# Kernel optimization log

Measured on AMD Instinct MI355X. Metric: run time of the kernel, lower is better.

## Reference

```python
import jax, jax.numpy as jnp
import numpy as np

N, E, C, NTT, NMOL = 200000, 1600000, 128, 20000, 2000
EPS = 1e-5


def setup_inputs() -> dict:
    key = jax.random.key(0)
    ks = jax.random.split(key, 32)
    s = 0.05
    d = {}
    d["node_attr"] = jax.random.normal(ks[0], (N, C), jnp.float32)
    d["adj_index"] = jax.random.randint(ks[1], (2, E), 0, N)
    d["adj_value"] = jax.random.uniform(ks[2], (E,), jnp.float32)
    d["tt_node_batch"] = jnp.sort(jax.random.randint(ks[3], (N,), 0, NTT))
    d["tt_graph_batch"] = jnp.sort(jax.random.randint(ks[4], (NTT,), 0, NMOL))
    # GCN layers (2): linear weight/bias
    d["W_gcn"] = jax.random.normal(ks[5], (2, C, C)) * s
    d["b_gcn"] = jnp.zeros((2, C))
    # 8 BatchNorm1d(C): [gcn0, gcn1, tt0, tt1, tt2, mol0, mol1, mol2] (eval mode)
    d["bn_gamma"] = jnp.ones((8, C))
    d["bn_beta"] = jnp.zeros((8, C))
    d["bn_mean"] = jnp.zeros((8, C))
    d["bn_var"] = jnp.ones((8, C))
    # 2 GATConv (tt, mol): bipartite lin_src/lin_dst, att_src/att_dst, bias (heads=1)
    d["gat_Wsrc"] = jax.random.normal(ks[6], (2, C, C)) * s
    d["gat_Wdst"] = jax.random.normal(ks[7], (2, C, C)) * s
    d["gat_asrc"] = jax.random.normal(ks[8], (2, C)) * s
    d["gat_adst"] = jax.random.normal(ks[9], (2, C)) * s
    d["gat_bias"] = jnp.zeros((2, C))
    # 2 GRUCell(C, C)
    d["gru_Wih"] = jax.random.normal(ks[10], (2, 3 * C, C)) * s
    d["gru_Whh"] = jax.random.normal(ks[11], (2, 3 * C, C)) * s
    d["gru_bih"] = jnp.zeros((2, 3 * C))
    d["gru_bhh"] = jnp.zeros((2, 3 * C))
    # predictor: 128 -> 64 (relu) -> 1
    d["pW1"] = jax.random.normal(ks[12], (64, C)) * s
    d["pb1"] = jnp.full((64,), 0.01)
    d["pW2"] = jax.random.normal(ks[13], (1, 64)) * s
    d["pb2"] = jnp.full((1,), 0.01)
    return d


def _bn(x, i, g, b, m, v):
    return (x - m[i]) * (g[i] / jnp.sqrt(v[i] + EPS)) + b[i]


def _spmm(idx, val, x, n):  # out[i] = sum_j A[i,j] x[j]
    return jax.ops.segment_sum(val[:, None] * x[idx[1]], idx[0], num_segments=n)


def _gat(x_src, x_dst, src, dst, nseg, Ws, Wd, a_s, a_d, bias):
    hs = x_src @ Ws.T
    hd = x_dst @ Wd.T
    alpha = jax.nn.leaky_relu(hs @ a_s, 0.01 * 0 + 0.01) if False else None
    a = (hs @ a_s)[src] + (hd @ a_d)[dst]
    a = jnp.where(a > 0, a, 0.01 * a)  # leaky_relu, negative_slope=0.01
    mx = jax.ops.segment_max(a, dst, num_segments=nseg)
    e = jnp.exp(a - mx[dst])
    den = jax.ops.segment_sum(e, dst, num_segments=nseg)
    w = e / den[dst]
    return jax.ops.segment_sum(w[:, None] * hs[src], dst, num_segments=nseg) + bias


def _gru(x, h, Wih, Whh, bih, bhh):
    gi = x @ Wih.T + bih
    gh = h @ Whh.T + bhh
    ir, iz, inn = jnp.split(gi, 3, axis=-1)
    hr, hz, hn = jnp.split(gh, 3, axis=-1)
    r = jax.nn.sigmoid(ir + hr)
    z = jax.nn.sigmoid(iz + hz)
    n = jnp.tanh(inn + r * hn)
    return (1.0 - z) * n + z * h


def _pool_stage(x, seg, nseg, bn_base, gi, bn_gamma, bn_beta, bn_mean, bn_var,
                gat_Wsrc, gat_Wdst, gat_asrc, gat_adst, gat_bias,
                gru_Wih, gru_Whh, gru_bih, gru_bhh):
    x = _bn(x, bn_base, bn_gamma, bn_beta, bn_mean, bn_var)
    mean = jax.ops.segment_sum(x, seg, num_segments=nseg)  # global_add_pool
    mean = _bn(jax.nn.relu(mean), bn_base + 1, bn_gamma, bn_beta, bn_mean, bn_var)
    src = jnp.arange(x.shape[0])
    g = _gat(x, mean, src, seg, nseg, gat_Wsrc[gi], gat_Wdst[gi], gat_asrc[gi], gat_adst[gi], gat_bias[gi])
    g = jax.nn.elu(g)  # dropout p=0.001 is identity in eval
    g = _gru(g, mean, gru_Wih[gi], gru_Whh[gi], gru_bih[gi], gru_bhh[gi])
    return _bn(jax.nn.relu(g), bn_base + 2, bn_gamma, bn_beta, bn_mean, bn_var)


def reference(node_attr, adj_value, W_gcn, b_gcn, bn_gamma, bn_beta, bn_mean, bn_var,
              gat_Wsrc, gat_Wdst, gat_asrc, gat_adst, gat_bias,
              gru_Wih, gru_Whh, gru_bih, gru_bhh, pW1, pb1, pW2, pb2,
              adj_index, tt_node_batch, tt_graph_batch):
    # graph embedder: two GCN layers  x <- relu(BN(A @ (x W^T) + b))
    x = node_attr
    for i in range(2):
        x = _spmm(adj_index, adj_value, x @ W_gcn[i].T, N) + b_gcn[i]
        x = jax.nn.relu(_bn(x, i, bn_gamma, bn_beta, bn_mean, bn_var))
    # tt pooling: nodes -> tt subgraphs
    tt = _pool_stage(x, tt_node_batch, NTT, 2, 0, bn_gamma, bn_beta, bn_mean, bn_var,
                     gat_Wsrc, gat_Wdst, gat_asrc, gat_adst, gat_bias,
                     gru_Wih, gru_Whh, gru_bih, gru_bhh)
    # mol pooling: tt subgraphs -> molecules
    mol = _pool_stage(tt, tt_graph_batch, NMOL, 5, 1, bn_gamma, bn_beta, bn_mean, bn_var,
                      gat_Wsrc, gat_Wdst, gat_asrc, gat_adst, gat_bias,
                      gru_Wih, gru_Whh, gru_bih, gru_bhh)
    # predictor
    h = jax.nn.relu(mol @ pW1.T + pb1)
    return h @ pW2.T + pb2  # [NMOL, 1]
```

## Files before the change

kernel.cpp:

```cpp
#include <hip/hip_runtime.h>
#include <math.h>

#define CCH 128
#define G3  384
#define BN_EPS 1e-5f
#define BSH 9
#define BROWS 512
#define COLBITS 19

typedef __bf16 bf16;
typedef __bf16 bf16x2 __attribute__((ext_vector_type(2)));
typedef __bf16 bf16x4 __attribute__((ext_vector_type(4)));
typedef __bf16 bf16x8 __attribute__((ext_vector_type(8)));
typedef float f32x4 __attribute__((ext_vector_type(4)));

__global__ __launch_bounds__(256) void prep_kernel(
    const float* __restrict__ g, const float* __restrict__ b,
    const float* __restrict__ m, const float* __restrict__ v,
    float* __restrict__ bnsc, float* __restrict__ bnsh,
    const float* __restrict__ Wsrc, const float* __restrict__ Wdst,
    const float* __restrict__ asrc, const float* __restrict__ adst,
    float* __restrict__ vsp, float* __restrict__ vd, float* __restrict__ c0,
    const int* __restrict__ tt_node_batch, int N, int NTT, int* __restrict__ starts_tt,
    const int* __restrict__ tt_graph_batch, int NMOL, int* __restrict__ starts_mol,
    int* __restrict__ bhist,
    const float* __restrict__ Wgcn, bf16* __restrict__ Wgcnb,
    bf16* __restrict__ Wsrcb,
    const float* __restrict__ Wih, bf16* __restrict__ Wihb,
    const float* __restrict__ Whh, bf16* __restrict__ Whhb,
    int B1, int B2, int B3, int B4, int B5, int B6, int B7, int B8)
{
    __shared__ float red[2];
    const int bid = blockIdx.x;
    const int tid = threadIdx.x;
    if (bid < B1) {
        int idx = bid * 256 + tid;
        if (idx < 8 * CCH) {
            float s = g[idx] / sqrtf(v[idx] + BN_EPS);
            bnsc[idx] = s;
            bnsh[idx] = b[idx] - m[idx] * s;
        }
    } else if (bid < B2) {
        int s = bid - B1;
        int which = tid >> 7, k = tid & 127;
        const float* W = (which ? Wdst : Wsrc) + s * CCH * CCH;
        const float* a = (which ? adst : asrc) + s * CCH;
        float acc = 0.f;
        for (int j = 0; j < CCH; ++j) acc += W[j * CCH + k] * a[j];
        if (which) {
            vd[s * CCH + k] = acc;
        } else {
            int l = 2 + 3 * s;
            float scl = g[l * CCH + k] / sqrtf(v[l * CCH + k] + BN_EPS);
            float shf = b[l * CCH + k] - m[l * CCH + k] * scl;
            vsp[s * CCH + k] = acc * scl;
            float p = shf * acc;
            for (int o = 32; o; o >>= 1) p += __shfl_down(p, o);
            if ((k & 63) == 0) red[k >> 6] = p;
        }
        __syncthreads();
        if (tid == 0) c0[s] = red[0] + red[1];
    } else if (bid < B3) {
        int s = (bid - B2) * 256 + tid;
        if (s <= NTT) {
            int lo = 0, hi = N;
            while (lo < hi) { int mid = (lo + hi) >> 1; if (tt_node_batch[mid] < s) lo = mid + 1; else hi = mid; }
            starts_tt[s] = lo;
        }
    } else if (bid < B4) {
        int s = (bid - B3) * 256 + tid;
        if (s <= NMOL) {
            int lo = 0, hi = NTT;
            while (lo < hi) { int mid = (lo + hi) >> 1; if (tt_graph_batch[mid] < s) lo = mid + 1; else hi = mid; }
            starts_mol[s] = lo;
        }
    } else if (bid < B5) {
        bhist[tid] = 0; bhist[tid + 256] = 0;
    } else {
        const float* src; bf16* dst; int u0;
        if (bid < B6)      { src = Wgcn; dst = Wgcnb; u0 = (bid - B5) * 256; }
        else if (bid < B7) { src = Wsrc; dst = Wsrcb; u0 = (bid - B6) * 256; }
        else if (bid < B8) { src = Wih;  dst = Wihb;  u0 = (bid - B7) * 256; }
        else               { src = Whh;  dst = Whhb;  u0 = (bid - B8) * 256; }
        int u = u0 + tid;
        int row = u >> 4, kc = u & 15;
        int bi = row >> 7, nrow = row & 127;
        const float* s = src + (size_t)row * CCH + kc * 8;
        float4 a = *(const float4*)s;
        float4 b4 = *(const float4*)(s + 4);
        bf16x8 o = { (bf16)a.x, (bf16)a.y, (bf16)a.z, (bf16)a.w,
                     (bf16)b4.x, (bf16)b4.y, (bf16)b4.z, (bf16)b4.w };
        *(bf16x8*)&dst[(size_t)bi * 16384 + ((kc * 128 + nrow) << 3)] = o;
    }
}


__global__ __launch_bounds__(256) void bucket_hist_kernel(const int* __restrict__ rows,
                                                          int* __restrict__ bhist, int E)
{
    __shared__ int h[512];
    int t = threadIdx.x;
    h[t] = 0; h[t + 256] = 0;
    __syncthreads();
    int base = blockIdx.x * 4096;
#pragma unroll
    for (int i = 0; i < 16; ++i) {
        int e = base + i * 256 + t;
        if (e < E) atomicAdd(&h[rows[e] >> BSH], 1);
    }
    __syncthreads();
    if (h[t]) atomicAdd(&bhist[t], h[t]);
    if (h[t + 256]) atomicAdd(&bhist[t + 256], h[t + 256]);
}

__global__ __launch_bounds__(256) void bucket_scan_kernel(const int* __restrict__ bhist,
                                                          int* __restrict__ boff, int* __restrict__ bcur,
                                                          int* __restrict__ row_ptr, int NB, int N, int E)
{
    __shared__ int h[512], sx[512], wt[4];
    int t = threadIdx.x;
    h[t] = bhist[t]; h[t + 256] = bhist[t + 256];
    __syncthreads();
    int v0 = h[2 * t], v1 = h[2 * t + 1];
    int s = v0 + v1, incl = s;
    for (int o = 1; o < 64; o <<= 1) { int u = __shfl_up(incl, o); if ((t & 63) >= o) incl += u; }
    if ((t & 63) == 63) wt[t >> 6] = incl;
    __syncthreads();
    int woff = 0, w = t >> 6;
    for (int i = 0; i < w; ++i) woff += wt[i];
    int excl = woff + incl - s;
    sx[2 * t] = excl; sx[2 * t + 1] = excl + v0;
    __syncthreads();
    if (t < NB)       { boff[t] = sx[t];       bcur[t] = sx[t]; }
    if (t + 256 < NB) { boff[t + 256] = sx[t + 256]; bcur[t + 256] = sx[t + 256]; }
    if (t == 0) { boff[NB] = E; row_ptr[N] = E; }
}

__global__ __launch_bounds__(256) void bucket_bin_kernel(
    const int* __restrict__ rows, const int* __restrict__ cols, const float* __restrict__ val,
    int* __restrict__ bcur, int2* __restrict__ bcv, int E)
{
    __shared__ int hist[512], sx[512], cnt[512], gbase[512], wt[4];
    __shared__ int mb[4096];
    __shared__ int2 mcv[4096];
    int t = threadIdx.x;
    hist[t] = 0; hist[t + 256] = 0; cnt[t] = 0; cnt[t + 256] = 0;
    __syncthreads();
    int base = blockIdx.x * 4096;
    int r[16];
#pragma unroll
    for (int i = 0; i < 16; ++i) {
        int e = base + i * 256 + t;
        r[i] = (e < E) ? rows[e] : -1;
        if (r[i] >= 0) atomicAdd(&hist[r[i] >> BSH], 1);
    }
    __syncthreads();
    int v0 = hist[2 * t], v1 = hist[2 * t + 1];
    int s = v0 + v1, incl = s;
    for (int o = 1; o < 64; o <<= 1) { int u = __shfl_up(incl, o); if ((t & 63) >= o) incl += u; }
    if ((t & 63) == 63) wt[t >> 6] = incl;
    __syncthreads();
    int woff = 0, w = t >> 6;
    for (int i = 0; i < w; ++i) woff += wt[i];
    int excl = woff + incl - s;
    sx[2 * t] = excl; sx[2 * t + 1] = excl + v0;
    __syncthreads();
    for (int bb = t; bb < 512; bb += 256)
        if (hist[bb]) gbase[bb] = atomicAdd(&bcur[bb], hist[bb]);
    __syncthreads();
#pragma unroll
    for (int i = 0; i < 16; ++i) {
        if (r[i] < 0) continue;
        int e = base + i * 256 + t;
        int bb = r[i] >> BSH;
        int p = atomicAdd(&cnt[bb], 1);
        int loc = sx[bb] + p;
        mb[loc] = bb;
        int2 cv;
        cv.x = cols[e] | ((r[i] & (BROWS - 1)) << COLBITS);
        cv.y = __float_as_int(val[e]);
        mcv[loc] = cv;
    }
    __syncthreads();
    int Mv = sx[511] + hist[511];
    for (int loc = t; loc < Mv; loc += 256) {
        int bb = mb[loc];
        int gidx = gbase[bb] + (loc - sx[bb]);
        bcv[gidx] = mcv[loc];
    }
}

__global__ __launch_bounds__(256) void bucket_place_kernel(
    const int2* __restrict__ bcv, const int* __restrict__ boff, int* __restrict__ row_ptr,
    int2* __restrict__ cpack, int N)
{
    __shared__ int rcnt[512], sx[512], wt[4];
    int b = blockIdx.x;
    int t = threadIdx.x;
    rcnt[t] = 0; rcnt[t + 256] = 0;
    __syncthreads();
    int rbase = b << BSH;
    int rn = min(BROWS, N - rbase);
    int lo = boff[b], hi = boff[b + 1];
    for (int p = lo + t; p < hi; p += 256)
        atomicAdd(&rcnt[((unsigned)bcv[p].x) >> COLBITS], 1);
    __syncthreads();
    int v0 = rcnt[2 * t], v1 = rcnt[2 * t + 1];
    int s = v0 + v1, incl = s;
    for (int o = 1; o < 64; o <<= 1) { int u = __shfl_up(incl, o); if ((t & 63) >= o) incl += u; }
    if ((t & 63) == 63) wt[t >> 6] = incl;
    __syncthreads();
    int woff = 0, w = t >> 6;
    for (int i = 0; i < w; ++i) woff += wt[i];
    int excl = woff + incl - s;
    sx[2 * t] = excl; sx[2 * t + 1] = excl + v0;
    __syncthreads();
    if (t < rn)       row_ptr[rbase + t] = lo + sx[t];
    if (t + 256 < rn) row_ptr[rbase + t + 256] = lo + sx[t + 256];
    __syncthreads();
    sx[t] += lo; sx[t + 256] += lo;
    __syncthreads();
    for (int p = lo + t; p < hi; p += 256) {
        int2 cv = bcv[p];
        int rin = ((unsigned)cv.x) >> COLBITS;
        int slot = atomicAdd(&sx[rin], 1);
        cv.x &= (1 << COLBITS) - 1;
        cpack[slot] = cv;
    }
}


template<int IN_BF16, int OUT_BF16, int ACT>
__global__ __launch_bounds__(256, 4) void gemm_mfma(
    const void* __restrict__ Xv, const bf16* __restrict__ Wf,
    const float* __restrict__ bias, void* __restrict__ Yv, int M, int Nout)
{
    __shared__ bf16 Xs[128 * 128];
    const int tid = threadIdx.x;
    const int rb = blockIdx.x * 128;
    const int cb = blockIdx.y * 128;
    const bf16* Wfb = Wf + (size_t)cb * CCH;

    if (IN_BF16) {
#pragma unroll
        for (int i = 0; i < 8; ++i) {
            int c = tid + i * 256;
            int r = c >> 4, kc = c & 15;
            int grow = rb + r;
            bf16x8 o = {};
            if (grow < M) o = *(const bf16x8*)&((const bf16*)Xv)[(size_t)grow * CCH + kc * 8];
            *(bf16x8*)&Xs[(r * 16 + (kc ^ (r & 15))) << 3] = o;
        }
    } else {
#pragma unroll
        for (int i = 0; i < 16; ++i) {
            int c = tid + i * 256;
            int r = c >> 5, sub = c & 31;
            int kc = sub >> 1, half = sub & 1;
            int grow = rb + r;
            bf16x4 o = {};
            if (grow < M) {
                float4 xv = *(const float4*)&((const float*)Xv)[(size_t)grow * CCH + kc * 8 + half * 4];
                o[0] = (bf16)xv.x; o[1] = (bf16)xv.y; o[2] = (bf16)xv.z; o[3] = (bf16)xv.w;
            }
            *(bf16x4*)&Xs[((r * 16 + (kc ^ (r & 15))) << 3) + half * 4] = o;
        }
    }
    __syncthreads();

    const int w = tid >> 6, lane = tid & 63;
    const int col16 = lane & 15, quad = lane >> 4;
    const int wm = (w & 1) * 64, wn = (w >> 1) * 64;

    f32x4 acc[4][4] = {};
#pragma unroll
    for (int kk = 0; kk < 4; ++kk) {
        const int kc = kk * 4 + quad;
        bf16x8 bfr[4], af[4];
#pragma unroll
        for (int ni = 0; ni < 4; ++ni)
            bfr[ni] = *(const bf16x8*)&Wfb[(size_t)((kc * 128 + wn + ni * 16 + col16) << 3)];
#pragma unroll
        for (int mi = 0; mi < 4; ++mi) {
            int r = wm + mi * 16 + col16;
            af[mi] = *(const bf16x8*)&Xs[(r * 16 + (kc ^ col16)) << 3];
        }
#pragma unroll
        for (int mi = 0; mi < 4; ++mi)
#pragma unroll
            for (int ni = 0; ni < 4; ++ni)
                acc[mi][ni] = __builtin_amdgcn_mfma_f32_16x16x32_bf16(af[mi], bfr[ni], acc[mi][ni], 0, 0, 0);
    }

#pragma unroll
    for (int mi = 0; mi < 4; ++mi) {
#pragma unroll
        for (int r = 0; r < 4; ++r) {
            int row = rb + wm + mi * 16 + quad * 4 + r;
            if (row >= M) continue;
#pragma unroll
            for (int ni = 0; ni < 4; ++ni) {
                int col = cb + wn + ni * 16 + col16;
                float vv = acc[mi][ni][r];
                if (bias) vv += bias[col];
                if (ACT == 1) vv = vv > 0.f ? vv : expm1f(vv);
                if (OUT_BF16) ((bf16*)Yv)[(size_t)row * Nout + col] = (bf16)vv;
                else          ((float*)Yv)[(size_t)row * Nout + col] = vv;
            }
        }
    }
}

__global__ __launch_bounds__(256, 4) void gemm_dual(
    const float* __restrict__ X0, const bf16* __restrict__ W0,
    const float* __restrict__ b0, float* __restrict__ Y0,
    const float* __restrict__ X1, const bf16* __restrict__ W1,
    const float* __restrict__ b1, float* __restrict__ Y1, int M)
{
    __shared__ bf16 Xs[128 * 128];
    const int tid = threadIdx.x;
    const int rb = blockIdx.x * 128;
    const int yy = blockIdx.y;
    const float* X; const bf16* W; const float* bias; float* Y; int cb;
    if (yy < 3) { X = X0; W = W0; bias = b0; Y = Y0; cb = yy * 128; }
    else        { X = X1; W = W1; bias = b1; Y = Y1; cb = (yy - 3) * 128; }
    const bf16* Wfb = W + (size_t)cb * CCH;

#pragma unroll
    for (int i = 0; i < 16; ++i) {
        int c = tid + i * 256;
        int r = c >> 5, sub = c & 31;
        int kc = sub >> 1, half = sub & 1;
        int grow = rb + r;
        bf16x4 o = {};
        if (grow < M) {
            float4 xv = *(const float4*)&X[(size_t)grow * CCH + kc * 8 + half * 4];
            o[0] = (bf16)xv.x; o[1] = (bf16)xv.y; o[2] = (bf16)xv.z; o[3] = (bf16)xv.w;
        }
        *(bf16x4*)&Xs[((r * 16 + (kc ^ (r & 15))) << 3) + half * 4] = o;
    }
    __syncthreads();

    const int w = tid >> 6, lane = tid & 63;
    const int col16 = lane & 15, quad = lane >> 4;
    const int wm = (w & 1) * 64, wn = (w >> 1) * 64;

    f32x4 acc[4][4] = {};
#pragma unroll
    for (int kk = 0; kk < 4; ++kk) {
        const int kc = kk * 4 + quad;
        bf16x8 bfr[4], af[4];
#pragma unroll
        for (int ni = 0; ni < 4; ++ni)
            bfr[ni] = *(const bf16x8*)&Wfb[(size_t)((kc * 128 + wn + ni * 16 + col16) << 3)];
#pragma unroll
        for (int mi = 0; mi < 4; ++mi) {
            int r = wm + mi * 16 + col16;
            af[mi] = *(const bf16x8*)&Xs[(r * 16 + (kc ^ col16)) << 3];
        }
#pragma unroll
        for (int mi = 0; mi < 4; ++mi)
#pragma unroll
            for (int ni = 0; ni < 4; ++ni)
                acc[mi][ni] = __builtin_amdgcn_mfma_f32_16x16x32_bf16(af[mi], bfr[ni], acc[mi][ni], 0, 0, 0);
    }

#pragma unroll
    for (int mi = 0; mi < 4; ++mi) {
#pragma unroll
        for (int r = 0; r < 4; ++r) {
            int row = rb + wm + mi * 16 + quad * 4 + r;
            if (row >= M) continue;
#pragma unroll
            for (int ni = 0; ni < 4; ++ni) {
                int col = cb + wn + ni * 16 + col16;
                Y[(size_t)row * G3 + col] = acc[mi][ni][r] + bias[col];
            }
        }
    }
}

template<int SCORES>
__global__ __launch_bounds__(256) void spmm_csr_kernel(
    const int* __restrict__ row_ptr, const int2* __restrict__ cpack,
    const bf16* __restrict__ Xin, bf16* __restrict__ Y,
    const float* __restrict__ bvec, const float* __restrict__ sc, const float* __restrict__ sh,
    const float* __restrict__ vsp, const float* __restrict__ c0p, float* __restrict__ scores,
    int Nrow)
{
    int gid = blockIdx.x * 256 + threadIdx.x;
    int row = gid >> 4;
    if (row >= Nrow) return;
    int l8 = (gid & 15) << 3;
    int st = row_ptr[row], en = row_ptr[row + 1];
    float acc[8] = {};
    int j = st;
    for (; j + 4 <= en; j += 4) {
        int2 p0 = cpack[j], p1 = cpack[j + 1], p2 = cpack[j + 2], p3 = cpack[j + 3];
        bf16x8 x0 = *(const bf16x8*)&Xin[(size_t)p0.x * CCH + l8];
        bf16x8 x1 = *(const bf16x8*)&Xin[(size_t)p1.x * CCH + l8];
        bf16x8 x2 = *(const bf16x8*)&Xin[(size_t)p2.x * CCH + l8];
        bf16x8 x3 = *(const bf16x8*)&Xin[(size_t)p3.x * CCH + l8];
        float v0 = __int_as_float(p0.y), v1 = __int_as_float(p1.y);
        float v2 = __int_as_float(p2.y), v3 = __int_as_float(p3.y);
#pragma unroll
        for (int q = 0; q < 8; ++q)
            acc[q] += v0 * (float)x0[q] + v1 * (float)x1[q] + v2 * (float)x2[q] + v3 * (float)x3[q];
    }
    if (j + 2 <= en) {
        int2 p0 = cpack[j], p1 = cpack[j + 1];
        bf16x8 x0 = *(const bf16x8*)&Xin[(size_t)p0.x * CCH + l8];
        bf16x8 x1 = *(const bf16x8*)&Xin[(size_t)p1.x * CCH + l8];
        float v0 = __int_as_float(p0.y), v1 = __int_as_float(p1.y);
#pragma unroll
        for (int q = 0; q < 8; ++q) acc[q] += v0 * (float)x0[q] + v1 * (float)x1[q];
        j += 2;
    }
    if (j < en) {
        int2 p0 = cpack[j];
        bf16x8 x0 = *(const bf16x8*)&Xin[(size_t)p0.x * CCH + l8];
        float v0 = __int_as_float(p0.y);
#pragma unroll
        for (int q = 0; q < 8; ++q) acc[q] += v0 * (float)x0[q];
    }
    float o[8];
    bf16x8 ov;
#pragma unroll
    for (int q = 0; q < 8; ++q) {
        o[q] = fmaxf((acc[q] + bvec[l8 + q]) * sc[l8 + q] + sh[l8 + q], 0.f);
        ov[q] = (bf16)o[q];
    }
    *(bf16x8*)&Y[(size_t)row * CCH + l8] = ov;
    if (SCORES) {
        float p = 0.f;
#pragma unroll
        for (int q = 0; q < 8; ++q) p += o[q] * vsp[l8 + q];
        for (int d = 8; d; d >>= 1) p += __shfl_down(p, d, 16);
        if ((gid & 15) == 0) scores[row] = p + c0p[0];
    }
}

__global__ __launch_bounds__(128) void segstage_kernel(
    const bf16* __restrict__ X, const float* __restrict__ sarr, const int* __restrict__ starts,
    const float* __restrict__ sc2, const float* __restrict__ sh2,
    const float* __restrict__ sc3, const float* __restrict__ sh3,
    const float* __restrict__ vd, float* __restrict__ mean, float* __restrict__ upool)
{
    __shared__ float red[2];
    __shared__ float adsh;
    int t = blockIdx.x;
    int c = threadIdx.x;
    int st = starts[t], en = starts[t + 1];
    float sum = 0.f;
    for (int i = st; i < en; ++i) sum += (float)X[(size_t)i * CCH + c];
    float cnt = (float)(en - st);
    float poolb = fmaxf(sum * sc2[c] + cnt * sh2[c], 0.f);
    float mv = poolb * sc3[c] + sh3[c];
    mean[(size_t)t * CCH + c] = mv;
    float p = mv * vd[c];
    for (int o = 32; o; o >>= 1) p += __shfl_down(p, o);
    if ((c & 63) == 0) red[c >> 6] = p;
    __syncthreads();
    if (c == 0) adsh = red[0] + red[1];
    __syncthreads();
    if (en == st) { upool[(size_t)t * CCH + c] = 0.f; return; }
    float adt = adsh;
    float lm = -3.0e38f;
    for (int i = st + c; i < en; i += 128) {
        float a = sarr[i] + adt;
        a = a > 0.f ? a : 0.01f * a;
        lm = fmaxf(lm, a);
    }
    for (int o = 32; o; o >>= 1) lm = fmaxf(lm, __shfl_down(lm, o));
    if ((c & 63) == 0) red[c >> 6] = lm;
    __syncthreads();
    float m = fmaxf(red[0], red[1]);
    float u = 0.f, den = 0.f;
    for (int i = st; i < en; ++i) {
        float a = sarr[i] + adt;
        a = a > 0.f ? a : 0.01f * a;
        float e = __expf(a - m);
        den += e;
        u += e * (float)X[(size_t)i * CCH + c];
    }
    upool[(size_t)t * CCH + c] = (u / den) * sc2[c] + sh2[c];
}

__global__ __launch_bounds__(256) void gru_kernel(
    const float* __restrict__ giM, const float* __restrict__ ghM, const float* __restrict__ mean,
    const float* __restrict__ sc4, const float* __restrict__ sh4,
    bf16* __restrict__ out,
    const float* __restrict__ vsp2, const float* __restrict__ c02, float* __restrict__ scores,
    int total)
{
    __shared__ float sred[4];
    int idx = blockIdx.x * 256 + threadIdx.x;
    bool ok = idx < total;
    int t = idx >> 7, c = idx & 127;
    float o = 0.f;
    if (ok) {
        size_t b = (size_t)t * G3;
        float ir = giM[b + c],  iz = giM[b + 128 + c], inn = giM[b + 256 + c];
        float hr = ghM[b + c],  hz = ghM[b + 128 + c], hn  = ghM[b + 256 + c];
        float r = 1.f / (1.f + __expf(-(ir + hr)));
        float z = 1.f / (1.f + __expf(-(iz + hz)));
        float nn = tanhf(inn + r * hn);
        float h = (1.f - z) * nn + z * mean[idx];
        h = fmaxf(h, 0.f);
        o = h * sc4[c] + sh4[c];
        out[idx] = (bf16)o;
    }
    float p = ok ? o * vsp2[c] : 0.f;
    for (int d = 32; d; d >>= 1) p += __shfl_down(p, d);
    int w = threadIdx.x >> 6;
    if ((threadIdx.x & 63) == 0) sred[w] = p;
    __syncthreads();
    if (threadIdx.x == 0 && ok)   scores[t] = sred[0] + sred[1] + c02[0];
    if (threadIdx.x == 128 && ok) scores[t] = sred[2] + sred[3] + c02[0];
}

__global__ __launch_bounds__(256) void gru_pred_kernel(
    const float* __restrict__ giM, const float* __restrict__ ghM, const float* __restrict__ mean,
    const float* __restrict__ sc4, const float* __restrict__ sh4,
    const float* __restrict__ pW1, const float* __restrict__ pb1,
    const float* __restrict__ pW2, const float* __restrict__ pb2,
    float* __restrict__ out, int nseg)
{
    __shared__ float row[2][CCH];
    int half = threadIdx.x >> 7;
    int c = threadIdx.x & 127;
    int t = blockIdx.x * 2 + half;
    bool ok = t < nseg;
    float o = 0.f;
    if (ok) {
        size_t b = (size_t)t * G3;
        float ir = giM[b + c],  iz = giM[b + 128 + c], inn = giM[b + 256 + c];
        float hr = ghM[b + c],  hz = ghM[b + 128 + c], hn  = ghM[b + 256 + c];
        float r = 1.f / (1.f + __expf(-(ir + hr)));
        float z = 1.f / (1.f + __expf(-(iz + hz)));
        float nn = tanhf(inn + r * hn);
        float h = (1.f - z) * nn + z * mean[(size_t)t * CCH + c];
        h = fmaxf(h, 0.f);
        o = h * sc4[c] + sh4[c];
    }
    row[half][c] = o;
    __syncthreads();
    if (c < 64 && ok) {
        float h = pb1[c];
#pragma unroll
        for (int k = 0; k < CCH; ++k) h += row[half][k] * pW1[c * CCH + k];
        h = fmaxf(h, 0.f);
        float p = h * pW2[c];
        for (int d = 32; d; d >>= 1) p += __shfl_down(p, d);
        if (c == 0) out[t] = p + pb2[0];
    }
}


extern "C" void kernel_launch(void* const* d_in, const int* in_sizes, int n_in,
                              void* d_out, int out_size, void* d_ws, size_t ws_size,
                              hipStream_t stream)
{
    (void)n_in; (void)ws_size;
    const float* node_attr      = (const float*)d_in[0];
    const int*   adj_index      = (const int*)  d_in[1];
    const float* adj_value      = (const float*)d_in[2];
    const int*   tt_node_batch  = (const int*)  d_in[3];
    const int*   tt_graph_batch = (const int*)  d_in[4];
    const float* W_gcn    = (const float*)d_in[5];
    const float* b_gcn    = (const float*)d_in[6];
    const float* bn_gamma = (const float*)d_in[7];
    const float* bn_beta  = (const float*)d_in[8];
    const float* bn_mean  = (const float*)d_in[9];
    const float* bn_var   = (const float*)d_in[10];
    const float* gat_Wsrc = (const float*)d_in[11];
    const float* gat_Wdst = (const float*)d_in[12];
    const float* gat_asrc = (const float*)d_in[13];
    const float* gat_adst = (const float*)d_in[14];
    const float* gat_bias = (const float*)d_in[15];
    const float* gru_Wih  = (const float*)d_in[16];
    const float* gru_Whh  = (const float*)d_in[17];
    const float* gru_bih  = (const float*)d_in[18];
    const float* gru_bhh  = (const float*)d_in[19];
    const float* pW1 = (const float*)d_in[20];
    const float* pb1 = (const float*)d_in[21];
    const float* pW2 = (const float*)d_in[22];
    const float* pb2 = (const float*)d_in[23];

    const int E    = in_sizes[2];
    const int N    = in_sizes[3];
    const int NTT  = in_sizes[4];
    const int NMOL = out_size;
    const int NB   = (N + BROWS - 1) >> BSH;

    const int* adj_rows = adj_index;
    const int* adj_cols = adj_index + E;

    char* wsb = (char*)d_ws;
    size_t off = 0;
    auto carve = [&](size_t bytes) -> char* {
        char* p = wsb + off;
        off = (off + bytes + 255) & ~(size_t)255;
        return p;
    };
    bf16* bufB = (bf16*)carve((size_t)N * CCH * 2);
    bf16* bufA = (bf16*)carve((size_t)N * CCH * 2);
    bf16* tt   = (bf16*)carve((size_t)NTT * CCH * 2);
    float* mean  = (float*)carve((size_t)NTT * CCH * 4);
    float* upool = (float*)carve((size_t)NTT * CCH * 4);
    float* gbuf  = (float*)carve((size_t)NTT * CCH * 4);
    float* giM   = (float*)carve((size_t)NTT * G3 * 4);
    float* ghM   = (float*)carve((size_t)NTT * G3 * 4);
    float* scores = (float*)carve((size_t)N * 4);
    int* starts_tt  = (int*)carve((size_t)(NTT + 1) * 4);
    int* starts_mol = (int*)carve((size_t)(NMOL + 1) * 4);
    float* bnsc = (float*)carve(8 * CCH * 4);
    float* bnsh = (float*)carve(8 * CCH * 4);
    float* vsp  = (float*)carve(2 * CCH * 4);
    float* vd   = (float*)carve(2 * CCH * 4);
    float* c0   = (float*)carve(2 * 4);
    bf16* Wgcnb = (bf16*)carve((size_t)2 * CCH * CCH * 2);
    bf16* Wsrcb = (bf16*)carve((size_t)2 * CCH * CCH * 2);
    bf16* Wihb  = (bf16*)carve((size_t)2 * G3 * CCH * 2);
    bf16* Whhb  = (bf16*)carve((size_t)2 * G3 * CCH * 2);
    int*   bhist   = (int*)carve(512 * 4);
    int*   boff    = (int*)carve((size_t)(NB + 1) * 4);
    int*   bcur    = (int*)carve((size_t)NB * 4);
    int*   row_ptr = (int*)carve((size_t)(N + 1) * 4);
    int2*  bcv     = (int2*)carve((size_t)E * 8);
    int2*  cpack   = (int2*)carve((size_t)E * 8);

    const int B1 = 4;
    const int B2 = B1 + 2;
    const int B3 = B2 + (NTT + 1 + 255) / 256;
    const int B4 = B3 + (NMOL + 1 + 255) / 256;
    const int B5 = B4 + 1;
    const int B6 = B5 + 16;
    const int B7 = B6 + 16;
    const int B8 = B7 + 48;
    const int B9 = B8 + 48;
    prep_kernel<<<B9, 256, 0, stream>>>(
        bn_gamma, bn_beta, bn_mean, bn_var, bnsc, bnsh,
        gat_Wsrc, gat_Wdst, gat_asrc, gat_adst, vsp, vd, c0,
        tt_node_batch, N, NTT, starts_tt,
        tt_graph_batch, NMOL, starts_mol,
        bhist,
        W_gcn, Wgcnb, Wsrcb, gru_Wih, Wihb, gru_Whh, Whhb,
        B1, B2, B3, B4, B5, B6, B7, B8);

    const int nchunk = (E + 4095) / 4096;
    bucket_hist_kernel<<<nchunk, 256, 0, stream>>>(adj_rows, bhist, E);
    bucket_scan_kernel<<<1, 256, 0, stream>>>(bhist, boff, bcur, row_ptr, NB, N, E);
    bucket_bin_kernel<<<nchunk, 256, 0, stream>>>(adj_rows, adj_cols, adj_value, bcur, bcv, E);
    bucket_place_kernel<<<NB, 256, 0, stream>>>(bcv, boff, row_ptr, cpack, N);

    dim3 gg((N + 127) / 128, 1);
    const int spmm_blocks = ((size_t)N * 16 + 255) / 256;
    gemm_mfma<0, 1, 0><<<gg, 256, 0, stream>>>(node_attr, Wgcnb, nullptr, bufB, N, CCH);
    spmm_csr_kernel<0><<<spmm_blocks, 256, 0, stream>>>(
        row_ptr, cpack, bufB, bufA, b_gcn, bnsc, bnsh, nullptr, nullptr, nullptr, N);
    gemm_mfma<1, 1, 0><<<gg, 256, 0, stream>>>(bufA, Wgcnb + CCH * CCH, nullptr, bufB, N, CCH);
    spmm_csr_kernel<1><<<spmm_blocks, 256, 0, stream>>>(
        row_ptr, cpack, bufB, bufA, b_gcn + CCH, bnsc + CCH, bnsh + CCH,
        vsp, c0, scores, N);

    {
        const int bnb = 2, gi = 0, nseg = NTT;
        segstage_kernel<<<nseg, 128, 0, stream>>>(bufA, scores, starts_tt,
            bnsc + bnb * CCH, bnsh + bnb * CCH, bnsc + (bnb + 1) * CCH, bnsh + (bnb + 1) * CCH,
            vd + gi * CCH, mean, upool);
        dim3 g1((nseg + 127) / 128, 1);
        gemm_mfma<0, 0, 1><<<g1, 256, 0, stream>>>(upool, Wsrcb + gi * CCH * CCH,
                                                   gat_bias + gi * CCH, gbuf, nseg, CCH);
        dim3 g2((nseg + 127) / 128, 6);
        gemm_dual<<<g2, 256, 0, stream>>>(gbuf, Wihb + gi * G3 * CCH, gru_bih + gi * G3, giM,
                                          mean, Whhb + gi * G3 * CCH, gru_bhh + gi * G3, ghM, nseg);
        gru_kernel<<<(nseg * CCH + 255) / 256, 256, 0, stream>>>(giM, ghM, mean,
            bnsc + (bnb + 2) * CCH, bnsh + (bnb + 2) * CCH, tt,
            vsp + CCH, c0 + 1, scores, nseg * CCH);
    }

    {
        const int bnb = 5, gi = 1, nseg = NMOL;
        segstage_kernel<<<nseg, 128, 0, stream>>>(tt, scores, starts_mol,
            bnsc + bnb * CCH, bnsh + bnb * CCH, bnsc + (bnb + 1) * CCH, bnsh + (bnb + 1) * CCH,
            vd + gi * CCH, mean, upool);
        dim3 g1((nseg + 127) / 128, 1);
        gemm_mfma<0, 0, 1><<<g1, 256, 0, stream>>>(upool, Wsrcb + gi * CCH * CCH,
                                                   gat_bias + gi * CCH, gbuf, nseg, CCH);
        dim3 g2((nseg + 127) / 128, 6);
        gemm_dual<<<g2, 256, 0, stream>>>(gbuf, Wihb + gi * G3 * CCH, gru_bih + gi * G3, giM,
                                          mean, Whhb + gi * G3 * CCH, gru_bhh + gi * G3, ghM, nseg);
        gru_pred_kernel<<<(nseg + 1) / 2, 256, 0, stream>>>(giM, ghM, mean,
            bnsc + (bnb + 2) * CCH, bnsh + (bnb + 2) * CCH,
            pW1, pb1, pW2, pb2, (float*)d_out, nseg);
    }
}
```

Before: 595.4 us.

## Fuse GRU gate GEMMs with GRU elementwise epilogue and widen SpMM unroll

Replaces the dual GEMM plus separate GRU elementwise kernel with one kernel. Each block computes the r, n and z gate tiles for 64 rows in registers and applies the GRU update, batch norm and score dot-product directly, so the fp32 giM/ghM intermediates are never written to memory. The GAT pooled and projected buffers become bf16, and the predictor moves into its own small kernel. The SpMM inner loop is also unrolled to 8 neighbours per iteration to keep more gathers in flight, at the cost of higher register pressure.

```diff
diff --git a/kernel.cpp b/kernel.cpp
--- a/kernel.cpp
+++ b/kernel.cpp
@@ -311,72 +311,136 @@
     }
 }
 
-__global__ __launch_bounds__(256, 4) void gemm_dual(
-    const float* __restrict__ X0, const bf16* __restrict__ W0,
-    const float* __restrict__ b0, float* __restrict__ Y0,
-    const float* __restrict__ X1, const bf16* __restrict__ W1,
-    const float* __restrict__ b1, float* __restrict__ Y1, int M)
-{
-    __shared__ bf16 Xs[128 * 128];
+template<int TT>
+__global__ __launch_bounds__(256, 2) void gru_gemm_kernel(
+    const bf16* __restrict__ Agi, const float* __restrict__ meanf,
+    const bf16* __restrict__ Wih, const bf16* __restrict__ Whh,
+    const float* __restrict__ bih, const float* __restrict__ bhh,
+    const float* __restrict__ sc4, const float* __restrict__ sh4,
+    void* __restrict__ out,
+    const float* __restrict__ vsp2, const float* __restrict__ c02, float* __restrict__ scores,
+    int M)
+{
+    __shared__ bf16 Xi[64 * 128];
+    __shared__ bf16 Xh[64 * 128];
+    __shared__ float sred[64];
     const int tid = threadIdx.x;
-    const int rb = blockIdx.x * 128;
-    const int yy = blockIdx.y;
-    const float* X; const bf16* W; const float* bias; float* Y; int cb;
-    if (yy < 3) { X = X0; W = W0; bias = b0; Y = Y0; cb = yy * 128; }
-    else        { X = X1; W = W1; bias = b1; Y = Y1; cb = (yy - 3) * 128; }
-    const bf16* Wfb = W + (size_t)cb * CCH;
-
-#pragma unroll
-    for (int i = 0; i < 16; ++i) {
+    const int rb = blockIdx.x * 64;
+
+    if (TT && tid < 64) sred[tid] = 0.f;
+#pragma unroll
+    for (int i = 0; i < 4; ++i) {
+        int c = tid + i * 256;
+        int r = c >> 4, kc = c & 15;
+        int grow = rb + r;
+        bf16x8 o = {};
+        if (grow < M) o = *(const bf16x8*)&Agi[(size_t)grow * CCH + kc * 8];
+        *(bf16x8*)&Xi[(r * 16 + (kc ^ (r & 15))) << 3] = o;
+    }
+#pragma unroll
+    for (int i = 0; i < 8; ++i) {
         int c = tid + i * 256;
         int r = c >> 5, sub = c & 31;
         int kc = sub >> 1, half = sub & 1;
         int grow = rb + r;
         bf16x4 o = {};
         if (grow < M) {
-            float4 xv = *(const float4*)&X[(size_t)grow * CCH + kc * 8 + half * 4];
+            float4 xv = *(const float4*)&meanf[(size_t)grow * CCH + kc * 8 + half * 4];
             o[0] = (bf16)xv.x; o[1] = (bf16)xv.y; o[2] = (bf16)xv.z; o[3] = (bf16)xv.w;
         }
-        *(bf16x4*)&Xs[((r * 16 + (kc ^ (r & 15))) << 3) + half * 4] = o;
+        *(bf16x4*)&Xh[((r * 16 + (kc ^ (r & 15))) << 3) + half * 4] = o;
     }
     __syncthreads();
 
     const int w = tid >> 6, lane = tid & 63;
     const int col16 = lane & 15, quad = lane >> 4;
-    const int wm = (w & 1) * 64, wn = (w >> 1) * 64;
-
-    f32x4 acc[4][4] = {};
-#pragma unroll
-    for (int kk = 0; kk < 4; ++kk) {
-        const int kc = kk * 4 + quad;
-        bf16x8 bfr[4], af[4];
-#pragma unroll
-        for (int ni = 0; ni < 4; ++ni)
-            bfr[ni] = *(const bf16x8*)&Wfb[(size_t)((kc * 128 + wn + ni * 16 + col16) << 3)];
+
+    f32x4 carry[4][2];
+
+    const int phase_cb[3] = {0, 2, 1};
+#pragma unroll
+    for (int ph = 0; ph < 3; ++ph) {
+        const int cb = phase_cb[ph];
+        const bf16* Wi_t = Wih + (size_t)cb * 16384;
+        const bf16* Wh_t = Whh + (size_t)cb * 16384;
+        f32x4 ai[4][2] = {};
+        f32x4 ah[4][2] = {};
+#pragma unroll
+        for (int kk = 0; kk < 4; ++kk) {
+            const int kc = kk * 4 + quad;
+            bf16x8 bi_f[2], bh_f[2], xi_f[4], xh_f[4];
+#pragma unroll
+            for (int ni = 0; ni < 2; ++ni) {
+                int wc = w * 32 + ni * 16 + col16;
+                bi_f[ni] = *(const bf16x8*)&Wi_t[(size_t)((kc * 128 + wc) << 3)];
+                bh_f[ni] = *(const bf16x8*)&Wh_t[(size_t)((kc * 128 + wc) << 3)];
+            }
+#pragma unroll
+            for (int mi = 0; mi < 4; ++mi) {
+                int r = mi * 16 + col16;
+                xi_f[mi] = *(const bf16x8*)&Xi[(r * 16 + (kc ^ col16)) << 3];
+                xh_f[mi] = *(const bf16x8*)&Xh[(r * 16 + (kc ^ col16)) << 3];
+            }
+#pragma unroll
+            for (int mi = 0; mi < 4; ++mi)
+#pragma unroll
+                for (int ni = 0; ni < 2; ++ni) {
+                    ai[mi][ni] = __builtin_amdgcn_mfma_f32_16x16x32_bf16(xi_f[mi], bi_f[ni], ai[mi][ni], 0, 0, 0);
+                    ah[mi][ni] = __builtin_amdgcn_mfma_f32_16x16x32_bf16(xh_f[mi], bh_f[ni], ah[mi][ni], 0, 0, 0);
+                }
+        }
+        const int gofs = cb * 128;
 #pragma unroll
         for (int mi = 0; mi < 4; ++mi) {
-            int r = wm + mi * 16 + col16;
-            af[mi] = *(const bf16x8*)&Xs[(r * 16 + (kc ^ col16)) << 3];
-        }
-#pragma unroll
-        for (int mi = 0; mi < 4; ++mi)
-#pragma unroll
-            for (int ni = 0; ni < 4; ++ni)
-                acc[mi][ni] = __builtin_amdgcn_mfma_f32_16x16x32_bf16(af[mi], bfr[ni], acc[mi][ni], 0, 0, 0);
+#pragma unroll
+            for (int ni = 0; ni < 2; ++ni) {
+                int col = w * 32 + ni * 16 + col16;
+                float bi_v = bih[gofs + col], bh_v = bhh[gofs + col];
+#pragma unroll
+                for (int rr = 0; rr < 4; ++rr) {
+                    float vi = ai[mi][ni][rr] + bi_v;
+                    float vh = ah[mi][ni][rr] + bh_v;
+                    if (ph == 0) {
+                        carry[mi][ni][rr] = 1.f / (1.f + __expf(-(vi + vh)));
+                    } else if (ph == 1) {
+                        carry[mi][ni][rr] = tanhf(vi + carry[mi][ni][rr] * vh);
+                    } else {
+                        float z = 1.f / (1.f + __expf(-(vi + vh)));
+                        int row = rb + mi * 16 + quad * 4 + rr;
+                        float mval = (row < M) ? meanf[(size_t)row * CCH + col] : 0.f;
+                        float h = (1.f - z) * carry[mi][ni][rr] + z * mval;
+                        h = fmaxf(h, 0.f);
+                        float o = h * sc4[col] + sh4[col];
+                        carry[mi][ni][rr] = o;
+                    }
+                }
+            }
+        }
     }
 
 #pragma unroll
     for (int mi = 0; mi < 4; ++mi) {
 #pragma unroll
-        for (int r = 0; r < 4; ++r) {
-            int row = rb + wm + mi * 16 + quad * 4 + r;
-            if (row >= M) continue;
-#pragma unroll
-            for (int ni = 0; ni < 4; ++ni) {
-                int col = cb + wn + ni * 16 + col16;
-                Y[(size_t)row * G3 + col] = acc[mi][ni][r] + bias[col];
+        for (int rr = 0; rr < 4; ++rr) {
+            int rloc = mi * 16 + quad * 4 + rr;
+            int row = rb + rloc;
+            float p = 0.f;
+#pragma unroll
+            for (int ni = 0; ni < 2; ++ni) {
+                int col = w * 32 + ni * 16 + col16;
+                float o = carry[mi][ni][rr];
+                if (row < M) {
+                    if (TT) ((bf16*)out)[(size_t)row * CCH + col] = (bf16)o;
+                    else    ((float*)out)[(size_t)row * CCH + col] = o;
+                }
+                if (TT) p += o * vsp2[col];
             }
-        }
+            if (TT && row < M) atomicAdd(&sred[rloc], p);
+        }
+    }
+    if (TT) {
+        __syncthreads();
+        if (tid < 64 && rb + tid < M) scores[rb + tid] = sred[tid] + c02[0];
     }
 }
 
@@ -395,17 +459,32 @@
     int st = row_ptr[row], en = row_ptr[row + 1];
     float acc[8] = {};
     int j = st;
-    for (; j + 4 <= en; j += 4) {
-        int2 p0 = cpack[j], p1 = cpack[j + 1], p2 = cpack[j + 2], p3 = cpack[j + 3];
-        bf16x8 x0 = *(const bf16x8*)&Xin[(size_t)p0.x * CCH + l8];
-        bf16x8 x1 = *(const bf16x8*)&Xin[(size_t)p1.x * CCH + l8];
-        bf16x8 x2 = *(const bf16x8*)&Xin[(size_t)p2.x * CCH + l8];
-        bf16x8 x3 = *(const bf16x8*)&Xin[(size_t)p3.x * CCH + l8];
-        float v0 = __int_as_float(p0.y), v1 = __int_as_float(p1.y);
-        float v2 = __int_as_float(p2.y), v3 = __int_as_float(p3.y);
-#pragma unroll
-        for (int q = 0; q < 8; ++q)
-            acc[q] += v0 * (float)x0[q] + v1 * (float)x1[q] + v2 * (float)x2[q] + v3 * (float)x3[q];
+    for (; j + 8 <= en; j += 8) {
+        int2 p[8]; bf16x8 x[8];
+#pragma unroll
+        for (int u = 0; u < 8; ++u) p[u] = cpack[j + u];
+#pragma unroll
+        for (int u = 0; u < 8; ++u) x[u] = *(const bf16x8*)&Xin[(size_t)p[u].x * CCH + l8];
+#pragma unroll
+        for (int u = 0; u < 8; ++u) {
+            float vv = __int_as_float(p[u].y);
+#pragma unroll
+            for (int q = 0; q < 8; ++q) acc[q] += vv * (float)x[u][q];
+        }
+    }
+    if (j + 4 <= en) {
+        int2 p[4]; bf16x8 x[4];
+#pragma unroll
+        for (int u = 0; u < 4; ++u) p[u] = cpack[j + u];
+#pragma unroll
+        for (int u = 0; u < 4; ++u) x[u] = *(const bf16x8*)&Xin[(size_t)p[u].x * CCH + l8];
+#pragma unroll
+        for (int u = 0; u < 4; ++u) {
+            float vv = __int_as_float(p[u].y);
+#pragma unroll
+            for (int q = 0; q < 8; ++q) acc[q] += vv * (float)x[u][q];
+        }
+        j += 4;
     }
     if (j + 2 <= en) {
         int2 p0 = cpack[j], p1 = cpack[j + 1];
@@ -444,7 +523,7 @@
     const bf16* __restrict__ X, const float* __restrict__ sarr, const int* __restrict__ starts,
     const float* __restrict__ sc2, const float* __restrict__ sh2,
     const float* __restrict__ sc3, const float* __restrict__ sh3,
-    const float* __restrict__ vd, float* __restrict__ mean, float* __restrict__ upool)
+    const float* __restrict__ vd, float* __restrict__ mean, bf16* __restrict__ upool)
 {
     __shared__ float red[2];
     __shared__ float adsh;
@@ -463,7 +542,7 @@
     __syncthreads();
     if (c == 0) adsh = red[0] + red[1];
     __syncthreads();
-    if (en == st) { upool[(size_t)t * CCH + c] = 0.f; return; }
+    if (en == st) { upool[(size_t)t * CCH + c] = (bf16)0.f; return; }
     float adt = adsh;
     float lm = -3.0e38f;
     for (int i = st + c; i < en; i += 128) {
@@ -483,77 +562,26 @@
         den += e;
         u += e * (float)X[(size_t)i * CCH + c];
     }
-    upool[(size_t)t * CCH + c] = (u / den) * sc2[c] + sh2[c];
-}
-
-__global__ __launch_bounds__(256) void gru_kernel(
-    const float* __restrict__ giM, const float* __restrict__ ghM, const float* __restrict__ mean,
-    const float* __restrict__ sc4, const float* __restrict__ sh4,
-    bf16* __restrict__ out,
-    const float* __restrict__ vsp2, const float* __restrict__ c02, float* __restrict__ scores,
-    int total)
-{
-    __shared__ float sred[4];
-    int idx = blockIdx.x * 256 + threadIdx.x;
-    bool ok = idx < total;
-    int t = idx >> 7, c = idx & 127;
-    float o = 0.f;
-    if (ok) {
-        size_t b = (size_t)t * G3;
-        float ir = giM[b + c],  iz = giM[b + 128 + c], inn = giM[b + 256 + c];
-        float hr = ghM[b + c],  hz = ghM[b + 128 + c], hn  = ghM[b + 256 + c];
-        float r = 1.f / (1.f + __expf(-(ir + hr)));
-        float z = 1.f / (1.f + __expf(-(iz + hz)));
-        float nn = tanhf(inn + r * hn);
-        float h = (1.f - z) * nn + z * mean[idx];
-        h = fmaxf(h, 0.f);
-        o = h * sc4[c] + sh4[c];
-        out[idx] = (bf16)o;
-    }
-    float p = ok ? o * vsp2[c] : 0.f;
-    for (int d = 32; d; d >>= 1) p += __shfl_down(p, d);
-    int w = threadIdx.x >> 6;
-    if ((threadIdx.x & 63) == 0) sred[w] = p;
-    __syncthreads();
-    if (threadIdx.x == 0 && ok)   scores[t] = sred[0] + sred[1] + c02[0];
-    if (threadIdx.x == 128 && ok) scores[t] = sred[2] + sred[3] + c02[0];
-}
-
-__global__ __launch_bounds__(256) void gru_pred_kernel(
-    const float* __restrict__ giM, const float* __restrict__ ghM, const float* __restrict__ mean,
-    const float* __restrict__ sc4, const float* __restrict__ sh4,
-    const float* __restrict__ pW1, const float* __restrict__ pb1,
-    const float* __restrict__ pW2, const float* __restrict__ pb2,
-    float* __restrict__ out, int nseg)
-{
-    __shared__ float row[2][CCH];
-    int half = threadIdx.x >> 7;
-    int c = threadIdx.x & 127;
-    int t = blockIdx.x * 2 + half;
-    bool ok = t < nseg;
-    float o = 0.f;
-    if (ok) {
-        size_t b = (size_t)t * G3;
-        float ir = giM[b + c],  iz = giM[b + 128 + c], inn = giM[b + 256 + c];
-        float hr = ghM[b + c],  hz = ghM[b + 128 + c], hn  = ghM[b + 256 + c];
-        float r = 1.f / (1.f + __expf(-(ir + hr)));
-        float z = 1.f / (1.f + __expf(-(iz + hz)));
-        float nn = tanhf(inn + r * hn);
-        float h = (1.f - z) * nn + z * mean[(size_t)t * CCH + c];
-        h = fmaxf(h, 0.f);
-        o = h * sc4[c] + sh4[c];
-    }
-    row[half][c] = o;
-    __syncthreads();
-    if (c < 64 && ok) {
-        float h = pb1[c];
-#pragma unroll
-        for (int k = 0; k < CCH; ++k) h += row[half][k] * pW1[c * CCH + k];
-        h = fmaxf(h, 0.f);
-        float p = h * pW2[c];
-        for (int d = 32; d; d >>= 1) p += __shfl_down(p, d);
-        if (c == 0) out[t] = p + pb2[0];
-    }
+    upool[(size_t)t * CCH + c] = (bf16)((u / den) * sc2[c] + sh2[c]);
+}
+
+__global__ __launch_bounds__(64) void pred_kernel(
+    const float* __restrict__ mol, const float* __restrict__ pW1, const float* __restrict__ pb1,
+    const float* __restrict__ pW2, const float* __restrict__ pb2, float* __restrict__ out)
+{
+    __shared__ float row[CCH];
+    int m = blockIdx.x;
+    int j = threadIdx.x;
+    row[j] = mol[(size_t)m * CCH + j];
+    row[j + 64] = mol[(size_t)m * CCH + 64 + j];
+    __syncthreads();
+    float h = pb1[j];
+#pragma unroll
+    for (int k = 0; k < CCH; ++k) h += row[k] * pW1[j * CCH + k];
+    h = fmaxf(h, 0.f);
+    float p = h * pW2[j];
+    for (int o = 32; o; o >>= 1) p += __shfl_down(p, o);
+    if (j == 0) out[m] = p + pb2[0];
 }
 
 
@@ -606,11 +634,10 @@
     bf16* bufB = (bf16*)carve((size_t)N * CCH * 2);
     bf16* bufA = (bf16*)carve((size_t)N * CCH * 2);
     bf16* tt   = (bf16*)carve((size_t)NTT * CCH * 2);
+    float* mol  = (float*)carve((size_t)NMOL * CCH * 4);
     float* mean  = (float*)carve((size_t)NTT * CCH * 4);
-    float* upool = (float*)carve((size_t)NTT * CCH * 4);
-    float* gbuf  = (float*)carve((size_t)NTT * CCH * 4);
-    float* giM   = (float*)carve((size_t)NTT * G3 * 4);
-    float* ghM   = (float*)carve((size_t)NTT * G3 * 4);
+    bf16*  upool = (bf16*)carve((size_t)NTT * CCH * 2);
+    bf16*  gbuf  = (bf16*)carve((size_t)NTT * CCH * 2);
     float* scores = (float*)carve((size_t)N * 4);
     int* starts_tt  = (int*)carve((size_t)(NTT + 1) * 4);
     int* starts_mol = (int*)carve((size_t)(NMOL + 1) * 4);
@@ -670,14 +697,13 @@
             bnsc + bnb * CCH, bnsh + bnb * CCH, bnsc + (bnb + 1) * CCH, bnsh + (bnb + 1) * CCH,
             vd + gi * CCH, mean, upool);
         dim3 g1((nseg + 127) / 128, 1);
-        gemm_mfma<0, 0, 1><<<g1, 256, 0, stream>>>(upool, Wsrcb + gi * CCH * CCH,
+        gemm_mfma<1, 1, 1><<<g1, 256, 0, stream>>>(upool, Wsrcb + gi * CCH * CCH,
                                                    gat_bias + gi * CCH, gbuf, nseg, CCH);
-        dim3 g2((nseg + 127) / 128, 6);
-        gemm_dual<<<g2, 256, 0, stream>>>(gbuf, Wihb + gi * G3 * CCH, gru_bih + gi * G3, giM,
-                                          mean, Whhb + gi * G3 * CCH, gru_bhh + gi * G3, ghM, nseg);
-        gru_kernel<<<(nseg * CCH + 255) / 256, 256, 0, stream>>>(giM, ghM, mean,
-            bnsc + (bnb + 2) * CCH, bnsh + (bnb + 2) * CCH, tt,
-            vsp + CCH, c0 + 1, scores, nseg * CCH);
+        gru_gemm_kernel<1><<<(nseg + 63) / 64, 256, 0, stream>>>(
+            gbuf, mean, Wihb + gi * G3 * CCH, Whhb + gi * G3 * CCH,
+            gru_bih + gi * G3, gru_bhh + gi * G3,
+            bnsc + (bnb + 2) * CCH, bnsh + (bnb + 2) * CCH,
+            tt, vsp + CCH, c0 + 1, scores, nseg);
     }
 
     {
@@ -686,13 +712,13 @@
             bnsc + bnb * CCH, bnsh + bnb * CCH, bnsc + (bnb + 1) * CCH, bnsh + (bnb + 1) * CCH,
             vd + gi * CCH, mean, upool);
         dim3 g1((nseg + 127) / 128, 1);
-        gemm_mfma<0, 0, 1><<<g1, 256, 0, stream>>>(upool, Wsrcb + gi * CCH * CCH,
+        gemm_mfma<1, 1, 1><<<g1, 256, 0, stream>>>(upool, Wsrcb + gi * CCH * CCH,
                                                    gat_bias + gi * CCH, gbuf, nseg, CCH);
-        dim3 g2((nseg + 127) / 128, 6);
-        gemm_dual<<<g2, 256, 0, stream>>>(gbuf, Wihb + gi * G3 * CCH, gru_bih + gi * G3, giM,
-                                          mean, Whhb + gi * G3 * CCH, gru_bhh + gi * G3, ghM, nseg);
-        gru_pred_kernel<<<(nseg + 1) / 2, 256, 0, stream>>>(giM, ghM, mean,
+        gru_gemm_kernel<0><<<(nseg + 63) / 64, 256, 0, stream>>>(
+            gbuf, mean, Wihb + gi * G3 * CCH, Whhb + gi * G3 * CCH,
+            gru_bih + gi * G3, gru_bhh + gi * G3,
             bnsc + (bnb + 2) * CCH, bnsh + (bnb + 2) * CCH,
-            pW1, pb1, pW2, pb2, (float*)d_out, nseg);
-    }
-}
+            mol, nullptr, nullptr, nullptr, nseg);
+        pred_kernel<<<NMOL, 64, 0, stream>>>(mol, pW1, pb1, pW2, pb2, (float*)d_out);
+    }
+}
```

After: 618.9 us. 3.9% more time.
